# Optimization experiments

Measured on AMD Instinct MI355X. Metric: run time of the kernel, lower is better.

## Reference

```python
import jax, jax.numpy as jnp
import numpy as np

N_NODES = 100000
N_EDGES = 1600000
D_IN, D_HID, D_OUT = 32, 16, 2


def graph_conv(x, edge_index, w_rel, w_root, b):
    # PyG GraphConv (aggr='add'): out_i = x_i @ W_root^T + (sum_{j in N(i)} x_j) @ W_rel^T + b
    src, dst = edge_index[0], edge_index[1]
    msgs = x[src]                                            # [E, d] neighbor gather
    agg = jax.ops.segment_sum(msgs, dst, num_segments=N_NODES)  # [N, d] scatter-add
    return agg @ w_rel.T + x @ w_root.T + b


def setup_inputs() -> dict:
    key = jax.random.key(0)
    ks = jax.random.split(key, 8)
    x = jax.random.normal(ks[0], (N_NODES, D_IN), dtype=jnp.float32)
    edge_index = jax.random.randint(ks[1], (2, N_EDGES), 0, N_NODES, dtype=jnp.int64)
    def glorot(k, shape):
        lim = np.sqrt(6.0 / (shape[0] + shape[1]))
        return jax.random.uniform(k, shape, jnp.float32, -lim, lim)
    w1_rel = glorot(ks[2], (D_HID, D_IN))
    w1_root = glorot(ks[3], (D_HID, D_IN))
    b1 = jnp.zeros((D_HID,), jnp.float32)
    w2_rel = glorot(ks[4], (D_OUT, D_HID))
    w2_root = glorot(ks[5], (D_OUT, D_HID))
    b2 = jnp.zeros((D_OUT,), jnp.float32)
    return {"x": x, "edge_index": edge_index,
            "w1_rel": w1_rel, "w1_root": w1_root, "b1": b1,
            "w2_rel": w2_rel, "w2_root": w2_root, "b2": b2}


def reference(x, edge_index, w1_rel, w1_root, b1, w2_rel, w2_root, b2):
    h = graph_conv(x, edge_index, w1_rel, w1_root, b1)
    h = jax.nn.relu(h)
    out = graph_conv(h, edge_index, w2_rel, w2_root, b2)
    return out
```

## Files before the change

kernel.cpp:

```cpp
#include <hip/hip_runtime.h>

#define N_NODES 100000
#define N_EDGES 1600000
#define D_IN 32
#define D_HID 16
#define D_OUT 2

#define NPB 128
#define NB 782
#define NROWS (NB * NPB)
#define CHUNK 6400
#define BBLOCKS 250
#define EPT 13

#define PBC 2560
#define DUMMY_SRC 100000u
#define DUMMY_REC ((127u << 17) | DUMMY_SRC)
#define PAD_ALIGN 16

#define ACC2_K 16
#define ACC2_BPB 2
#define ACC2_BLOCKS (NB * ACC2_BPB)


__device__ __forceinline__ unsigned bfr(float x) {
    unsigned u = __float_as_uint(x);
    return (u + 0x7FFFu + ((u >> 16) & 1u)) >> 16;
}
__device__ __forceinline__ float bfu(unsigned lo16) {
    return __uint_as_float(lo16 << 16);
}

__global__ __launch_bounds__(512) void k_bin_node1(
    const int* __restrict__ ei, const float* __restrict__ x,
    const float* __restrict__ w_rel, const float* __restrict__ w_root,
    const float* __restrict__ bb,
    unsigned short* __restrict__ xr, float* __restrict__ agg,
    int* __restrict__ gcur, unsigned* __restrict__ recs2)
{
    __shared__ int cnt[NB];
    __shared__ int loff[NB];
    __shared__ int gbase[NB];
    __shared__ unsigned sorted[CHUNK];
    __shared__ unsigned short bkt16[CHUNK];
    __shared__ float s_rel[D_HID * D_IN];
    __shared__ float s_root[D_HID * D_IN];
    __shared__ float s_b[D_HID];
    int blk = blockIdx.x, tid = threadIdx.x;
    int e0 = blk * CHUNK;

    int srcs[EPT], dsts[EPT];
#pragma unroll
    for (int k = 0; k < EPT; k++) {
        int off = tid + k * 512;
        bool ok = off < CHUNK;
        int e = e0 + off;
        srcs[k] = ok ? ei[e] : 0;
        dsts[k] = ok ? ei[N_EDGES + e] : -1;
    }

    for (int i = tid; i < D_HID * D_IN; i += 512) {
        s_rel[i]  = w_rel[i];
        s_root[i] = w_root[i];
    }
    if (tid < D_HID) s_b[tid] = bb[tid];
    for (int i = tid; i < NB; i += 512) cnt[i] = 0;
    __syncthreads();

    int rank[EPT];
#pragma unroll
    for (int k = 0; k < EPT; k++)
        rank[k] = (dsts[k] >= 0) ? atomicAdd(&cnt[dsts[k] >> 7], 1) : 0;

    int node = blk * 512 + tid;
    if (node == N_NODES) {
        uint4* xp = (uint4*)(xr + (size_t)node * D_HID);
        xp[0] = make_uint4(0, 0, 0, 0);
        xp[1] = make_uint4(0, 0, 0, 0);
    } else if (node < N_NODES) {
        float row[D_IN];
        const float4* xp = (const float4*)(x + (size_t)node * D_IN);
#pragma unroll
        for (int i = 0; i < D_IN / 4; i++) {
            float4 v = xp[i];
            row[4*i+0] = v.x; row[4*i+1] = v.y; row[4*i+2] = v.z; row[4*i+3] = v.w;
        }
        float oa[D_HID], orr[D_HID];
#pragma unroll
        for (int o = 0; o < D_HID; o++) {
            float a = 0.f, r = s_b[o];
#pragma unroll
            for (int k = 0; k < D_IN; k++) {
                a += row[k] * s_rel[o * D_IN + k];
                r += row[k] * s_root[o * D_IN + k];
            }
            oa[o] = a; orr[o] = r;
        }
        unsigned p[8];
#pragma unroll
        for (int i = 0; i < 8; i++)
            p[i] = bfr(oa[2*i]) | (bfr(oa[2*i+1]) << 16);
        uint4* xrp = (uint4*)(xr + (size_t)node * D_HID);
        xrp[0] = make_uint4(p[0], p[1], p[2], p[3]);
        xrp[1] = make_uint4(p[4], p[5], p[6], p[7]);
        float4* aggp = (float4*)(agg + (size_t)node * D_HID);
#pragma unroll
        for (int i = 0; i < D_HID / 4; i++)
            aggp[i] = make_float4(orr[4*i], orr[4*i+1], orr[4*i+2], orr[4*i+3]);
    }
    __syncthreads();

    if (tid < 64) {
        int running = 0;
        for (int c = 0; c < (NB + 63) / 64; c++) {
            int idx = c * 64 + tid;
            int v = (idx < NB) ? cnt[idx] : 0;
            int incl = v;
#pragma unroll
            for (int off = 1; off < 64; off <<= 1) {
                int t = __shfl_up(incl, off);
                if (tid >= off) incl += t;
            }
            if (idx < NB) loff[idx] = running + incl - v;
            running += __shfl(incl, 63);
        }
    } else {
        for (int i = tid - 64; i < NB; i += 448)
            gbase[i] = (cnt[i] > 0) ? atomicAdd(&gcur[i], cnt[i]) : 0;
    }
    __syncthreads();

#pragma unroll
    for (int k = 0; k < EPT; k++) {
        if (dsts[k] >= 0) {
            int bkt = dsts[k] >> 7;
            int p = loff[bkt] + rank[k];
            sorted[p] = ((unsigned)(dsts[k] & (NPB - 1)) << 17) | (unsigned)srcs[k];
            bkt16[p] = (unsigned short)bkt;
        }
    }
    __syncthreads();

    for (int i = tid; i < CHUNK; i += 512) {
        int b = bkt16[i];
        int idx = gbase[b] + (i - loff[b]);
        if (idx < PBC)
            recs2[b * PBC + idx] = sorted[i];
    }
}

__global__ __launch_bounds__(512) void k_sortacc(
    const int* __restrict__ gcur, unsigned* __restrict__ recs2,
    const unsigned short* __restrict__ srcf, float* __restrict__ dstf,
    const float* __restrict__ w_rel2, const float* __restrict__ w_root2,
    const float* __restrict__ bb2,
    float* __restrict__ hr, float* __restrict__ outv)
{
    __shared__ unsigned stage[PBC];
    __shared__ unsigned sorted[PBC];
    __shared__ int hist[NPB], base[NPB];
    __shared__ float s_rel2[D_OUT * D_HID];
    __shared__ float s_root2[D_OUT * D_HID];
    __shared__ float s_b2[D_OUT];
    int b = blockIdx.x, tid = threadIdx.x;
    int n = min(gcur[b], PBC);
    unsigned* w = recs2 + (size_t)b * PBC;

    if (tid < D_OUT * D_HID) {
        s_rel2[tid]  = w_rel2[tid];
        s_root2[tid] = w_root2[tid];
    }
    if (tid < D_OUT) s_b2[tid] = bb2[tid];

    if (tid < NPB) hist[tid] = 0;
    for (int i = tid; i < n; i += 512) stage[i] = w[i];
    __syncthreads();

    unsigned rc[PBC / 512];
    int rk[PBC / 512];
#pragma unroll
    for (int j = 0; j < PBC / 512; j++) {
        int i = tid + j * 512;
        if (i < n) {
            rc[j] = stage[i];
            rk[j] = atomicAdd(&hist[rc[j] >> 17], 1);
        } else {
            rc[j] = DUMMY_REC; rk[j] = -1;
        }
    }
    __syncthreads();

    if (tid < 64) {
        int v0 = hist[tid], v1 = hist[tid + 64];
        int s0 = v0, s1 = v1;
#pragma unroll
        for (int off = 1; off < 64; off <<= 1) {
            int t0 = __shfl_up(s0, off);
            int t1 = __shfl_up(s1, off);
            if (tid >= off) { s0 += t0; s1 += t1; }
        }
        int tot0 = __shfl(s0, 63);
        base[tid]      = s0 - v0;
        base[tid + 64] = tot0 + s1 - v1;
    }
    __syncthreads();

#pragma unroll
    for (int j = 0; j < PBC / 512; j++) {
        if (rk[j] >= 0)
            sorted[base[rc[j] >> 17] + rk[j]] = rc[j];
    }
    int npad = (n + PAD_ALIGN - 1) & ~(PAD_ALIGN - 1);
    for (int i = n + tid; i < npad; i += 512) sorted[i] = DUMMY_REC;
    __syncthreads();

    for (int i = tid; i < npad; i += 512) w[i] = sorted[i];

    int g = tid >> 4;
    int f = tid & (D_HID - 1);
    int dbase = b * NPB;
    for (int bse = g * 16; bse < npad; bse += 32 * 16) {
        unsigned e[16];
#pragma unroll
        for (int k = 0; k < 16; k++) e[k] = sorted[bse + k];
        float v[16];
#pragma unroll
        for (int k = 0; k < 16; k++)
            v[k] = bfu(srcf[(e[k] & 0x1FFFF) * D_HID + f]);

        unsigned curd = e[0] >> 17;
        float acc = v[0];
#pragma unroll
        for (int k = 1; k < 16; k++) {
            unsigned dl = e[k] >> 17;
            if (dl == curd) {
                acc += v[k];
            } else {
                atomicAdd(&dstf[(dbase + curd) * D_HID + f], acc);
                curd = dl;
                acc = v[k];
            }
        }
        atomicAdd(&dstf[(dbase + curd) * D_HID + f], acc);
    }

    __syncthreads();
    if (tid < NPB) {
        int node = dbase + tid;
        if (node < N_NODES) {
            float h[D_HID];
            const float4* ap = (const float4*)(dstf + (size_t)node * D_HID);
#pragma unroll
            for (int i = 0; i < D_HID / 4; i++) {
                float4 vv = ap[i];
                h[4*i+0] = fmaxf(vv.x, 0.f); h[4*i+1] = fmaxf(vv.y, 0.f);
                h[4*i+2] = fmaxf(vv.z, 0.f); h[4*i+3] = fmaxf(vv.w, 0.f);
            }
            float o_rel[D_OUT], o_root[D_OUT];
#pragma unroll
            for (int o = 0; o < D_OUT; o++) {
                float a = 0.f, r = s_b2[o];
#pragma unroll
                for (int k = 0; k < D_HID; k++) {
                    a += h[k] * s_rel2[o * D_HID + k];
                    r += h[k] * s_root2[o * D_HID + k];
                }
                o_rel[o] = a; o_root[o] = r;
            }
            ((float2*)hr)[node]   = make_float2(o_rel[0], o_rel[1]);
            ((float2*)outv)[node] = make_float2(o_root[0], o_root[1]);
        } else if (node == N_NODES) {
            ((float2*)hr)[node] = make_float2(0.f, 0.f);
        }
    }
}

__global__ __launch_bounds__(256) void k_acc2(
    const unsigned* __restrict__ recs2, const int* __restrict__ gcur,
    const float* __restrict__ hr, float* __restrict__ outv)
{
    int bucket = blockIdx.x / ACC2_BPB;
    int blk    = blockIdx.x % ACC2_BPB;
    int g = threadIdx.x >> 1;
    int f = threadIdx.x & 1;
    int r0 = (blk * 128 + g) * ACC2_K;
    int n = min(gcur[bucket], PBC);
    if (r0 >= n) return;
    const unsigned* rp = recs2 + (size_t)bucket * PBC + r0;

    unsigned e[ACC2_K];
#pragma unroll
    for (int k = 0; k < ACC2_K; k++) e[k] = rp[k];
    float v[ACC2_K];
#pragma unroll
    for (int k = 0; k < ACC2_K; k++)
        v[k] = hr[(e[k] & 0x1FFFF) * D_OUT + f];

    int dbase = bucket * NPB;
    unsigned cur = e[0] >> 17;
    float acc = v[0];
#pragma unroll
    for (int k = 1; k < ACC2_K; k++) {
        unsigned dl = e[k] >> 17;
        if (dl == cur) {
            acc += v[k];
        } else {
            int d = dbase + (int)cur;
            if (d < N_NODES) atomicAdd(&outv[d * D_OUT + f], acc);
            cur = dl;
            acc = v[k];
        }
    }
    int d = dbase + (int)cur;
    if (d < N_NODES) atomicAdd(&outv[d * D_OUT + f], acc);
}

extern "C" void kernel_launch(void* const* d_in, const int* in_sizes, int n_in,
                              void* d_out, int out_size, void* d_ws, size_t ws_size,
                              hipStream_t stream) {
    const float* x       = (const float*)d_in[0];
    const int*   ei      = (const int*)  d_in[1];
    const float* w1_rel  = (const float*)d_in[2];
    const float* w1_root = (const float*)d_in[3];
    const float* b1      = (const float*)d_in[4];
    const float* w2_rel  = (const float*)d_in[5];
    const float* w2_root = (const float*)d_in[6];
    const float* b2      = (const float*)d_in[7];
    float* out = (float*)d_out;

    float*          agg   = (float*)d_ws;
    unsigned short* xrh   = (unsigned short*)(agg + (size_t)NROWS * D_HID);
    unsigned*       recs2 = (unsigned*)(xrh + (size_t)NROWS * D_HID);
    float*          hr    = (float*)(recs2 + (size_t)NB * PBC);
    int*            gcur  = (int*)(hr + (size_t)NROWS * D_OUT);

    hipMemsetAsync(gcur, 0, NB * sizeof(int), stream);

    k_bin_node1<<<dim3(BBLOCKS), dim3(512), 0, stream>>>(
        ei, x, w1_rel, w1_root, b1, xrh, agg, gcur, recs2);

    k_sortacc<<<dim3(NB), dim3(512), 0, stream>>>(
        gcur, recs2, xrh, agg, w2_rel, w2_root, b2, hr, out);

    k_acc2<<<dim3(ACC2_BLOCKS), dim3(256), 0, stream>>>(recs2, gcur, hr, out);
}
```

Baseline: 152.0 us.

## Replace atomic segmented scatter with per-node CSR gather in both aggregation passes

After the in-block counting sort, each destination node's edges are now contiguous, so both layers switch from 16-edge segments with atomicAdd to a direct per-node gather. Four threads per node each own four features in layer 1, and two threads per node in layer 2. Per-node offsets and counts go into a new bbase array so the second kernel can find each node's segment, and outputs are written with a plain += instead of atomics. This removes atomic traffic and the padding records, but load balance now depends on node degree, and the per-node inner loop is divergent.

```diff
diff --git a/kernel.cpp b/kernel.cpp
--- a/kernel.cpp
+++ b/kernel.cpp
@@ -16,11 +16,6 @@
 #define PBC 2560
 #define DUMMY_SRC 100000u
 #define DUMMY_REC ((127u << 17) | DUMMY_SRC)
-#define PAD_ALIGN 16
-
-#define ACC2_K 16
-#define ACC2_BPB 2
-#define ACC2_BLOCKS (NB * ACC2_BPB)
 
 
 __device__ __forceinline__ unsigned bfr(float x) {
@@ -151,10 +146,11 @@
 
 __global__ __launch_bounds__(512) void k_sortacc(
     const int* __restrict__ gcur, unsigned* __restrict__ recs2,
-    const unsigned short* __restrict__ srcf, float* __restrict__ dstf,
+    const unsigned short* __restrict__ srcf, const float* __restrict__ agg,
     const float* __restrict__ w_rel2, const float* __restrict__ w_root2,
     const float* __restrict__ bb2,
-    float* __restrict__ hr, float* __restrict__ outv)
+    float* __restrict__ hr, float* __restrict__ outv,
+    unsigned* __restrict__ bbase)
 {
     __shared__ unsigned stage[PBC];
     __shared__ unsigned sorted[PBC];
@@ -210,65 +206,56 @@
         if (rk[j] >= 0)
             sorted[base[rc[j] >> 17] + rk[j]] = rc[j];
     }
-    int npad = (n + PAD_ALIGN - 1) & ~(PAD_ALIGN - 1);
-    for (int i = n + tid; i < npad; i += 512) sorted[i] = DUMMY_REC;
-    __syncthreads();
-
-    for (int i = tid; i < npad; i += 512) w[i] = sorted[i];
-
-    int g = tid >> 4;
-    int f = tid & (D_HID - 1);
-    int dbase = b * NPB;
-    for (int bse = g * 16; bse < npad; bse += 32 * 16) {
-        unsigned e[16];
-#pragma unroll
-        for (int k = 0; k < 16; k++) e[k] = sorted[bse + k];
-        float v[16];
-#pragma unroll
-        for (int k = 0; k < 16; k++)
-            v[k] = bfu(srcf[(e[k] & 0x1FFFF) * D_HID + f]);
-
-        unsigned curd = e[0] >> 17;
-        float acc = v[0];
-#pragma unroll
-        for (int k = 1; k < 16; k++) {
-            unsigned dl = e[k] >> 17;
-            if (dl == curd) {
-                acc += v[k];
-            } else {
-                atomicAdd(&dstf[(dbase + curd) * D_HID + f], acc);
-                curd = dl;
-                acc = v[k];
-            }
-        }
-        atomicAdd(&dstf[(dbase + curd) * D_HID + f], acc);
-    }
-
-    __syncthreads();
-    if (tid < NPB) {
-        int node = dbase + tid;
+    __syncthreads();
+
+    for (int i = tid; i < n; i += 512) w[i] = sorted[i];
+    if (tid < NPB)
+        bbase[b * NPB + tid] = (unsigned)base[tid] | ((unsigned)hist[tid] << 16);
+
+    int t = tid >> 2, l = tid & 3;
+    int node = b * NPB + t;
+    int cbase = base[t], c = hist[t];
+    float acc0, acc1, acc2_, acc3;
+    if (node < N_NODES) {
+        const float4 r4 = *(const float4*)(agg + (size_t)node * D_HID + l * 4);
+        acc0 = r4.x; acc1 = r4.y; acc2_ = r4.z; acc3 = r4.w;
+    } else {
+        acc0 = acc1 = acc2_ = acc3 = 0.f;
+    }
+    for (int r0 = 0; r0 < c; r0 += 8) {
+        int m = c - r0;
+        uint2 vv[8];
+#pragma unroll
+        for (int j = 0; j < 8; j++) {
+            unsigned src = (j < m) ? (sorted[cbase + r0 + j] & 0x1FFFF) : DUMMY_SRC;
+            vv[j] = *(const uint2*)(srcf + (size_t)src * D_HID + l * 4);
+        }
+#pragma unroll
+        for (int j = 0; j < 8; j++) {
+            acc0 += bfu(vv[j].x & 0xFFFFu); acc1 += bfu(vv[j].x >> 16);
+            acc2_ += bfu(vv[j].y & 0xFFFFu); acc3 += bfu(vv[j].y >> 16);
+        }
+    }
+
+    float h0 = fmaxf(acc0, 0.f), h1 = fmaxf(acc1, 0.f);
+    float h2 = fmaxf(acc2_, 0.f), h3 = fmaxf(acc3, 0.f);
+    float pr[D_OUT], pp[D_OUT];
+#pragma unroll
+    for (int o = 0; o < D_OUT; o++) {
+        const float* wr = &s_rel2[o * D_HID + l * 4];
+        const float* wo = &s_root2[o * D_HID + l * 4];
+        pr[o] = h0 * wr[0] + h1 * wr[1] + h2 * wr[2] + h3 * wr[3];
+        pp[o] = h0 * wo[0] + h1 * wo[1] + h2 * wo[2] + h3 * wo[3];
+    }
+#pragma unroll
+    for (int m = 1; m < 4; m <<= 1) {
+        pr[0] += __shfl_xor(pr[0], m); pr[1] += __shfl_xor(pr[1], m);
+        pp[0] += __shfl_xor(pp[0], m); pp[1] += __shfl_xor(pp[1], m);
+    }
+    if (l == 0) {
         if (node < N_NODES) {
-            float h[D_HID];
-            const float4* ap = (const float4*)(dstf + (size_t)node * D_HID);
-#pragma unroll
-            for (int i = 0; i < D_HID / 4; i++) {
-                float4 vv = ap[i];
-                h[4*i+0] = fmaxf(vv.x, 0.f); h[4*i+1] = fmaxf(vv.y, 0.f);
-                h[4*i+2] = fmaxf(vv.z, 0.f); h[4*i+3] = fmaxf(vv.w, 0.f);
-            }
-            float o_rel[D_OUT], o_root[D_OUT];
-#pragma unroll
-            for (int o = 0; o < D_OUT; o++) {
-                float a = 0.f, r = s_b2[o];
-#pragma unroll
-                for (int k = 0; k < D_HID; k++) {
-                    a += h[k] * s_rel2[o * D_HID + k];
-                    r += h[k] * s_root2[o * D_HID + k];
-                }
-                o_rel[o] = a; o_root[o] = r;
-            }
-            ((float2*)hr)[node]   = make_float2(o_rel[0], o_rel[1]);
-            ((float2*)outv)[node] = make_float2(o_root[0], o_root[1]);
+            ((float2*)hr)[node]   = make_float2(pr[0], pr[1]);
+            ((float2*)outv)[node] = make_float2(pp[0] + s_b2[0], pp[1] + s_b2[1]);
         } else if (node == N_NODES) {
             ((float2*)hr)[node] = make_float2(0.f, 0.f);
         }
@@ -276,43 +263,36 @@
 }
 
 __global__ __launch_bounds__(256) void k_acc2(
-    const unsigned* __restrict__ recs2, const int* __restrict__ gcur,
+    const unsigned* __restrict__ recs2, const unsigned* __restrict__ bbase,
     const float* __restrict__ hr, float* __restrict__ outv)
 {
-    int bucket = blockIdx.x / ACC2_BPB;
-    int blk    = blockIdx.x % ACC2_BPB;
-    int g = threadIdx.x >> 1;
-    int f = threadIdx.x & 1;
-    int r0 = (blk * 128 + g) * ACC2_K;
-    int n = min(gcur[bucket], PBC);
-    if (r0 >= n) return;
-    const unsigned* rp = recs2 + (size_t)bucket * PBC + r0;
-
-    unsigned e[ACC2_K];
-#pragma unroll
-    for (int k = 0; k < ACC2_K; k++) e[k] = rp[k];
-    float v[ACC2_K];
-#pragma unroll
-    for (int k = 0; k < ACC2_K; k++)
-        v[k] = hr[(e[k] & 0x1FFFF) * D_OUT + f];
-
-    int dbase = bucket * NPB;
-    unsigned cur = e[0] >> 17;
-    float acc = v[0];
-#pragma unroll
-    for (int k = 1; k < ACC2_K; k++) {
-        unsigned dl = e[k] >> 17;
-        if (dl == cur) {
-            acc += v[k];
-        } else {
-            int d = dbase + (int)cur;
-            if (d < N_NODES) atomicAdd(&outv[d * D_OUT + f], acc);
-            cur = dl;
-            acc = v[k];
-        }
-    }
-    int d = dbase + (int)cur;
-    if (d < N_NODES) atomicAdd(&outv[d * D_OUT + f], acc);
+    __shared__ unsigned srt[PBC];
+    int b = blockIdx.x, tid = threadIdx.x;
+    unsigned pk127 = bbase[b * NPB + 127];
+    int n = (int)(pk127 & 0xFFFFu) + (int)(pk127 >> 16);
+    const unsigned* rp = recs2 + (size_t)b * PBC;
+    for (int i = tid; i < n; i += 256) srt[i] = rp[i];
+
+    int t = tid >> 1, l = tid & 1;
+    unsigned pk = bbase[b * NPB + t];
+    int cbase = (int)(pk & 0xFFFFu), c = (int)(pk >> 16);
+    int node = b * NPB + t;
+    __syncthreads();
+
+    float acc = 0.f;
+    for (int r0 = 0; r0 < c; r0 += 8) {
+        int m = c - r0;
+        float vv[8];
+#pragma unroll
+        for (int j = 0; j < 8; j++) {
+            unsigned src = (j < m) ? (srt[cbase + r0 + j] & 0x1FFFF) : DUMMY_SRC;
+            vv[j] = hr[(size_t)src * D_OUT + l];
+        }
+#pragma unroll
+        for (int j = 0; j < 8; j++) acc += vv[j];
+    }
+    if (node < N_NODES)
+        outv[(size_t)node * D_OUT + l] += acc;
 }
 
 extern "C" void kernel_launch(void* const* d_in, const int* in_sizes, int n_in,
@@ -332,7 +312,8 @@
     unsigned short* xrh   = (unsigned short*)(agg + (size_t)NROWS * D_HID);
     unsigned*       recs2 = (unsigned*)(xrh + (size_t)NROWS * D_HID);
     float*          hr    = (float*)(recs2 + (size_t)NB * PBC);
-    int*            gcur  = (int*)(hr + (size_t)NROWS * D_OUT);
+    unsigned*       bbase = (unsigned*)(hr + (size_t)NROWS * D_OUT);
+    int*            gcur  = (int*)(bbase + (size_t)NROWS);
 
     hipMemsetAsync(gcur, 0, NB * sizeof(int), stream);
 
@@ -340,7 +321,7 @@
         ei, x, w1_rel, w1_root, b1, xrh, agg, gcur, recs2);
 
     k_sortacc<<<dim3(NB), dim3(512), 0, stream>>>(
-        gcur, recs2, xrh, agg, w2_rel, w2_root, b2, hr, out);
-
-    k_acc2<<<dim3(ACC2_BLOCKS), dim3(256), 0, stream>>>(recs2, gcur, hr, out);
-}
+        gcur, recs2, xrh, agg, w2_rel, w2_root, b2, hr, out, bbase);
+
+    k_acc2<<<dim3(NB), dim3(256), 0, stream>>>(recs2, bbase, hr, out);
+}
```

Result: faster. 134.9 us (-11.3%).
